# Optimization experiments

Hardware: AMD Instinct MI355X
Metric: run time of the kernel (lower is better)

## Reference

```python
import jax, jax.numpy as jnp
import numpy as np

B, S, D, M, E, K = 4, 1024, 2048, 512, 8, 2
AUX_W = 0.01


def setup_inputs() -> dict:
    key = jax.random.key(0)
    ks = jax.random.split(key, 9)
    n = lambda k, sh, fan: jax.random.normal(k, sh, jnp.float32) * (fan ** -0.5)
    return {
        "hidden_states": jax.random.normal(ks[0], (B, S, D), jnp.float32),
        "w_router": n(ks[1], (D, E), D),
        "wi0": n(ks[2], (E, D, M), D),
        "wi1": n(ks[3], (E, D, M), D),
        "wo": n(ks[4], (E, M, D), M),
        "sw_wi0": n(ks[5], (D, M), D),
        "sw_wi1": n(ks[6], (D, M), D),
        "sw_wo": n(ks[7], (M, D), M),
        "w_shared_gate": n(ks[8], (D, 1), D),
        "deterministic": 1,
    }


def reference(hidden_states, w_router, wi0, wi1, wo, sw_wi0, sw_wi1, sw_wo, w_shared_gate, deterministic):
    b, s, d = hidden_states.shape
    x = hidden_states.reshape(-1, d)  # [T, D]
    T = x.shape[0]

    # --- router: softmax over experts, top-k, renormalize top-k weights ---
    logits = (x @ w_router).astype(jnp.float32)           # [T, E]
    probs = jax.nn.softmax(logits, axis=-1)
    top_w, top_i = jax.lax.top_k(probs, K)                # [T, K]
    top_w = top_w / jnp.sum(top_w, axis=-1, keepdims=True)
    one_hot = jax.nn.one_hot(top_i, E, dtype=probs.dtype)  # [T, K, E]
    combine = jnp.einsum("tk,tke->te", top_w, one_hot)     # [T, E] sparse combine weights

    # --- load-balance aux loss (MaxText style) ---
    density = jnp.mean(jnp.sum(one_hot, axis=1), axis=0)    # fraction routed per expert
    density_proxy = jnp.mean(probs, axis=0)                 # mean router prob per expert
    load_balance_loss = jnp.mean(density * density_proxy) * (E * E) * AUX_W

    # --- routed experts: scan over experts, gated MLP, weighted combine ---
    def expert_step(acc, packed):
        wi0_e, wi1_e, wo_e, w_e = packed  # [D,M],[D,M],[M,D],[T]
        h = jax.nn.silu(x @ wi0_e) * (x @ wi1_e)            # [T, M]
        return acc + w_e[:, None] * (h @ wo_e), None

    routed, _ = jax.lax.scan(
        expert_step, jnp.zeros_like(x), (wi0, wi1, wo, combine.T)
    )

    # --- shared expert (gated MLP) + sigmoid shared gate ---
    hs = jax.nn.silu(x @ sw_wi0) * (x @ sw_wi1)
    shared = hs @ sw_wo                                     # [T, D]
    gate = jax.nn.sigmoid(x @ w_shared_gate)                # [T, 1]

    out = (routed + gate * shared).reshape(b, s, d)
    return out, load_balance_loss
```

## Files before the change

### kernel.cpp

```cpp
#include <hip/hip_runtime.h>
#include <hip/hip_bf16.h>
#include <math.h>

#define TT 4096
#define DD 2048
#define MM 512
#define EE 8

typedef __attribute__((ext_vector_type(8))) short short8;
typedef __attribute__((ext_vector_type(4))) float f32x4;

__device__ __forceinline__ unsigned short f2bf(float f) {
  union { float f; unsigned u; } v; v.f = f;
  unsigned u = v.u;
  unsigned r = u + 0x7FFFu + ((u >> 16) & 1u);
  return (unsigned short)(r >> 16);
}

__device__ __forceinline__ float bf2f(unsigned short u) {
  union { unsigned u; float f; } v; v.u = ((unsigned)u) << 16;
  return v.f;
}

__device__ __forceinline__ int imin(int a, int b) { return a < b ? a : b; }

__device__ __forceinline__ void gld16(const void* g, void* l) {
  __builtin_amdgcn_global_load_lds(
      (const __attribute__((address_space(1))) void*)g,
      (__attribute__((address_space(3))) void*)l, 16, 0, 0);
}

__global__ __launch_bounds__(256) void prep_kernel(
    const float* __restrict__ wi0, const float* __restrict__ wi1,
    const float* __restrict__ wo, const float* __restrict__ swi0,
    const float* __restrict__ swi1, const float* __restrict__ swo,
    unsigned short* __restrict__ wi0T, unsigned short* __restrict__ wi1T,
    unsigned short* __restrict__ woT, unsigned short* __restrict__ swi0T,
    unsigned short* __restrict__ swi1T, unsigned short* __restrict__ swoT,
    const float* __restrict__ x, const float* __restrict__ wr,
    const float* __restrict__ wg, unsigned short* __restrict__ xb,
    int* __restrict__ topk_i, float* __restrict__ topk_w,
    float* __restrict__ gate, int* __restrict__ cnt, float* __restrict__ proxy)
{
  __shared__ unsigned short st[64][72];
  __shared__ float s_proxy[EE];
  __shared__ int s_cnt[EE];
  int b = blockIdx.x;
  int tid = threadIdx.x;

  if (b < 27 * 64) {
    int slice = b >> 6, q = b & 63;
    const float* s; unsigned short* d;
    int R, C, tcb;
    if (slice < 8)       { s = wi0 + (size_t)slice * DD * MM;        d = wi0T + (size_t)slice * DD * MM;        R = DD; C = MM; tcb = 3; }
    else if (slice < 16) { s = wi1 + (size_t)(slice - 8) * DD * MM;  d = wi1T + (size_t)(slice - 8) * DD * MM;  R = DD; C = MM; tcb = 3; }
    else if (slice < 24) { s = wo + (size_t)(slice - 16) * MM * DD;  d = woT + (size_t)(slice - 16) * MM * DD;  R = MM; C = DD; tcb = 5; }
    else if (slice == 24){ s = swi0; d = swi0T; R = DD; C = MM; tcb = 3; }
    else if (slice == 25){ s = swi1; d = swi1T; R = DD; C = MM; tcb = 3; }
    else                 { s = swo;  d = swoT;  R = MM; C = DD; tcb = 5; }
    int ncmask = (1 << tcb) - 1;
    int tr = tid >> 4;
    int tc4 = (tid & 15) * 4;
    int orow = tid >> 2;
    int oc = (tid & 3) * 16;

    float4 cur[4], nxt[4];
    int t0 = q * 4;
    int c0 = (t0 & ncmask) * 64, r0 = (t0 >> tcb) * 64;
#pragma unroll
    for (int i = 0; i < 4; ++i)
      cur[i] = *(const float4*)&s[(size_t)(r0 + tr + i * 16) * C + (c0 + tc4)];

    for (int k = 0; k < 4; ++k) {
      int nr0 = 0, nc0 = 0;
      if (k < 3) {
        int t = q * 4 + k + 1;
        nc0 = (t & ncmask) * 64; nr0 = (t >> tcb) * 64;
#pragma unroll
        for (int i = 0; i < 4; ++i)
          nxt[i] = *(const float4*)&s[(size_t)(nr0 + tr + i * 16) * C + (nc0 + tc4)];
      }
      __builtin_amdgcn_s_barrier();
#pragma unroll
      for (int i = 0; i < 4; ++i) {
        int r = tr + i * 16;
        st[r][tc4 + 0] = f2bf(cur[i].x); st[r][tc4 + 1] = f2bf(cur[i].y);
        st[r][tc4 + 2] = f2bf(cur[i].z); st[r][tc4 + 3] = f2bf(cur[i].w);
      }
      asm volatile("s_waitcnt lgkmcnt(0)" ::: "memory");
      __builtin_amdgcn_s_barrier();
      short8 v0, v1;
#pragma unroll
      for (int j = 0; j < 8; ++j) { v0[j] = st[oc + j][orow]; v1[j] = st[oc + 8 + j][orow]; }
      *(short8*)&d[(size_t)(c0 + orow) * R + (r0 + oc)] = v0;
      *(short8*)&d[(size_t)(c0 + orow) * R + (r0 + oc + 8)] = v1;
      if (k < 3) {
        r0 = nr0; c0 = nc0;
#pragma unroll
        for (int i = 0; i < 4; ++i) cur[i] = nxt[i];
      }
    }
    return;
  }

  int rb = b - 27 * 64;
  if (tid < EE) { s_proxy[tid] = 0.f; s_cnt[tid] = 0; }
  __syncthreads();
  int wave = tid >> 6, lane = tid & 63;
  int t = rb * 4 + wave;
  const float* xr = x + (size_t)t * DD;
  unsigned short* xbr = xb + (size_t)t * DD;
  float p[EE];
#pragma unroll
  for (int e = 0; e < EE; ++e) p[e] = 0.f;
  float pg = 0.f;
  for (int i = 0; i < DD / 64; ++i) {
    int d = lane + i * 64;
    float xv = xr[d];
    xbr[d] = f2bf(xv);
    const float* w = wr + d * EE;
#pragma unroll
    for (int e = 0; e < EE; ++e) p[e] = fmaf(xv, w[e], p[e]);
    pg = fmaf(xv, wg[d], pg);
  }
#pragma unroll
  for (int e = 0; e < EE; ++e) {
#pragma unroll
    for (int off = 32; off; off >>= 1) p[e] += __shfl_xor(p[e], off);
  }
#pragma unroll
  for (int off = 32; off; off >>= 1) pg += __shfl_xor(pg, off);

  if (lane == 0) {
    float mx = p[0];
#pragma unroll
    for (int e = 1; e < EE; ++e) mx = fmaxf(mx, p[e]);
    float pr[EE]; float s = 0.f;
#pragma unroll
    for (int e = 0; e < EE; ++e) { pr[e] = __expf(p[e] - mx); s += pr[e]; }
    float inv = 1.f / s;
#pragma unroll
    for (int e = 0; e < EE; ++e) pr[e] *= inv;
    int i0 = 0;
#pragma unroll
    for (int e = 1; e < EE; ++e) if (p[e] > p[i0]) i0 = e;
    int i1 = (i0 == 0) ? 1 : 0;
#pragma unroll
    for (int e = 0; e < EE; ++e) if (e != i0 && p[e] > p[i1]) i1 = e;
    float w0 = pr[i0], w1 = pr[i1], s2 = w0 + w1;
    topk_i[t * 2] = i0; topk_i[t * 2 + 1] = i1;
    topk_w[t * 2] = w0 / s2; topk_w[t * 2 + 1] = w1 / s2;
    gate[t] = 1.f / (1.f + __expf(-pg));
    atomicAdd(&s_cnt[i0], 1);
    atomicAdd(&s_cnt[i1], 1);
#pragma unroll
    for (int e = 0; e < EE; ++e) atomicAdd(&s_proxy[e], pr[e]);
  }
  __syncthreads();
  if (tid < EE) {
    atomicAdd(&cnt[tid], s_cnt[tid]);
    atomicAdd(&proxy[tid], s_proxy[tid]);
  }
}

__global__ void offsets_loss_kernel(const int* __restrict__ cnt, int* __restrict__ offs,
                                    const float* __restrict__ proxy, float* __restrict__ out_loss)
{
  if (threadIdx.x == 0 && blockIdx.x == 0) {
    int acc = 0; float l = 0.f;
    for (int e = 0; e < EE; ++e) {
      offs[e] = acc; acc += cnt[e];
      l += (float)cnt[e] * proxy[e];
    }
    out_loss[0] = l * (0.01f * (float)EE) / ((float)TT * (float)TT);
  }
}

__global__ void fill_kernel(const int* __restrict__ topk_i,
                            const int* __restrict__ offs, int* __restrict__ fillc,
                            int* __restrict__ btok, int* __restrict__ slotOf)
{
  int idx = blockIdx.x * blockDim.x + threadIdx.x;
  if (idx >= TT * 2) return;
  int e = topk_i[idx];
  int slot = atomicAdd(&fillc[e], 1);
  int p = offs[e] + slot;
  btok[p] = idx >> 1;
  slotOf[idx] = p;
}

__global__ __launch_bounds__(256) void gemm1_kernel(
    const unsigned short* __restrict__ xb,
    const unsigned short* __restrict__ wi0T, const unsigned short* __restrict__ wi1T,
    const unsigned short* __restrict__ swi0T, const unsigned short* __restrict__ swi1T,
    unsigned short* __restrict__ H, unsigned short* __restrict__ Hs,
    const int* __restrict__ btok, const int* __restrict__ cnt, const int* __restrict__ offs)
{
  __shared__ __align__(16) unsigned short lA0[128 * 64];
  __shared__ __align__(16) unsigned short lA1[128 * 64];
  __shared__ __align__(16) unsigned short lB0[128 * 64];
  __shared__ __align__(16) unsigned short lB1[128 * 64];
  int z = blockIdx.z;
  const unsigned short *w0, *w1;
  const int* tok = nullptr;
  unsigned short* Ho;
  int n;
  if (z < EE) {
    n = cnt[z];
    int rb = offs[z];
    tok = btok + rb;
    w0 = wi0T + (size_t)z * (DD * MM);
    w1 = wi1T + (size_t)z * (DD * MM);
    Ho = H + (size_t)rb * MM;
  } else { n = TT; w0 = swi0T; w1 = swi1T; Ho = Hs; }
  int row0 = blockIdx.y * 128;
  if (row0 >= n) return;
  int m0 = blockIdx.x * 64;
  int tid = threadIdx.x, lane = tid & 63, wv = tid >> 6;

  int lsub = lane >> 3;
  int chl = (lane & 7) ^ lsub;

  const unsigned short* gA[4];
  const unsigned short* gB[4];
#pragma unroll
  for (int c = 0; c < 4; ++c) {
    int row = c * 32 + wv * 8 + lsub;
    int tr;
    if (tok) tr = tok[imin(row0 + row, n - 1)];
    else     tr = row0 + row;
    gA[c] = xb + (size_t)tr * DD + chl * 8;
    int mat = row >> 6, col = row & 63;
    const unsigned short* wsel = mat ? w1 : w0;
    gB[c] = wsel + (size_t)(m0 + col) * DD + chl * 8;
  }

  int rw = (wv & 1) * 64;
  int cg = (wv >> 1) * 32;
  int fr = lane & 15;
  int grp = lane >> 4;
  int lr4 = (lane >> 4) * 4, lc = lane & 15;

  f32x4 acc[4][4];
  f32x4 zf = {0.f, 0.f, 0.f, 0.f};
#pragma unroll
  for (int i = 0; i < 4; ++i)
#pragma unroll
    for (int c = 0; c < 4; ++c) acc[i][c] = zf;

  auto stage = [&](int kk, unsigned short* la, unsigned short* lb) {
#pragma unroll
    for (int c = 0; c < 4; ++c) gld16(gA[c] + kk, la + c * 2048 + wv * 512);
#pragma unroll
    for (int c = 0; c < 4; ++c) gld16(gB[c] + kk, lb + c * 2048 + wv * 512);
  };
  auto compute = [&](const unsigned short* la, const unsigned short* lb) {
#pragma unroll
    for (int s = 0; s < 2; ++s) {
      int cq = s * 4 + grp;
      short8 af[4], bf[4];
#pragma unroll
      for (int i = 0; i < 4; ++i) {
        int row = rw + i * 16 + fr;
        af[i] = *(const short8*)&la[row * 64 + ((cq ^ (row & 7)) * 8)];
      }
#pragma unroll
      for (int c = 0; c < 4; ++c) {
        int rowb = (c >> 1) * 64 + cg + (c & 1) * 16 + fr;
        bf[c] = *(const short8*)&lb[rowb * 64 + ((cq ^ (rowb & 7)) * 8)];
      }
#pragma unroll
      for (int i = 0; i < 4; ++i)
#pragma unroll
        for (int c = 0; c < 4; ++c)
          acc[i][c] = __builtin_amdgcn_mfma_f32_16x16x32_bf16(af[i], bf[c], acc[i][c], 0, 0, 0);
    }
  };

  stage(0, lA0, lB0);
  __syncthreads();

  int k0 = 0;
  for (; k0 < DD - 128; k0 += 128) {
    stage(k0 + 64, lA1, lB1);
    compute(lA0, lB0);
    __syncthreads();
    stage(k0 + 128, lA0, lB0);
    compute(lA1, lB1);
    __syncthreads();
  }
  stage(k0 + 64, lA1, lB1);
  compute(lA0, lB0);
  __syncthreads();
  compute(lA1, lB1);

#pragma unroll
  for (int i = 0; i < 4; ++i) {
#pragma unroll
    for (int c = 0; c < 2; ++c) {
#pragma unroll
      for (int rg = 0; rg < 4; ++rg) {
        int row = row0 + rw + i * 16 + lr4 + rg;
        if (row < n) {
          float a0 = acc[i][c][rg];
          float a1 = acc[i][c + 2][rg];
          float h = a0 / (1.f + __expf(-a0)) * a1;
          Ho[(size_t)row * MM + m0 + cg + c * 16 + lc] = f2bf(h);
        }
      }
    }
  }
}

__global__ __launch_bounds__(256) void gemm2_kernel(
    const unsigned short* __restrict__ H, const unsigned short* __restrict__ Hs,
    const unsigned short* __restrict__ woT, const unsigned short* __restrict__ swoT,
    unsigned short* __restrict__ Yr, unsigned short* __restrict__ Ys,
    const int* __restrict__ cnt, const int* __restrict__ offs)
{
  __shared__ __align__(16) unsigned short lA0[128 * 64];
  __shared__ __align__(16) unsigned short lA1[128 * 64];
  __shared__ __align__(16) unsigned short lB0[128 * 64];
  __shared__ __align__(16) unsigned short lB1[128 * 64];
  int z = blockIdx.z;
  int n, rb;
  const unsigned short *Hb, *wb;
  unsigned short* Yd;
  if (z < EE) { n = cnt[z]; rb = offs[z]; Hb = H + (size_t)rb * MM; wb = woT + (size_t)z * (DD * MM); Yd = Yr + (size_t)rb * DD; }
  else        { n = TT; rb = 0; Hb = Hs; wb = swoT; Yd = Ys; }
  int row0 = blockIdx.y * 128;
  if (row0 >= n) return;
  int d0 = blockIdx.x * 128;
  int tid = threadIdx.x, lane = tid & 63, wv = tid >> 6;

  int lsub = lane >> 3;
  int chl = (lane & 7) ^ lsub;

  const unsigned short* gA[4];
  const unsigned short* gB[4];
#pragma unroll
  for (int c = 0; c < 4; ++c) {
    int row = c * 32 + wv * 8 + lsub;
    int sr = imin(row0 + row, n - 1);
    gA[c] = Hb + (size_t)sr * MM + chl * 8;
    gB[c] = wb + (size_t)(d0 + row) * MM + chl * 8;
  }

  int rw = (wv & 1) * 64;
  int cw = (wv >> 1) * 64;
  int fr = lane & 15;
  int grp = lane >> 4;
  int lr4 = (lane >> 4) * 4, lc = lane & 15;

  f32x4 acc[4][4];
  f32x4 zf = {0.f, 0.f, 0.f, 0.f};
#pragma unroll
  for (int i = 0; i < 4; ++i)
#pragma unroll
    for (int c = 0; c < 4; ++c) acc[i][c] = zf;

  auto stage = [&](int kk, unsigned short* la, unsigned short* lb) {
#pragma unroll
    for (int c = 0; c < 4; ++c) gld16(gA[c] + kk, la + c * 2048 + wv * 512);
#pragma unroll
    for (int c = 0; c < 4; ++c) gld16(gB[c] + kk, lb + c * 2048 + wv * 512);
  };
  auto compute = [&](const unsigned short* la, const unsigned short* lb) {
#pragma unroll
    for (int s = 0; s < 2; ++s) {
      int cq = s * 4 + grp;
      short8 af[4], bf[4];
#pragma unroll
      for (int i = 0; i < 4; ++i) {
        int row = rw + i * 16 + fr;
        af[i] = *(const short8*)&la[row * 64 + ((cq ^ (row & 7)) * 8)];
      }
#pragma unroll
      for (int c = 0; c < 4; ++c) {
        int rowb = cw + c * 16 + fr;
        bf[c] = *(const short8*)&lb[rowb * 64 + ((cq ^ (rowb & 7)) * 8)];
      }
#pragma unroll
      for (int i = 0; i < 4; ++i)
#pragma unroll
        for (int c = 0; c < 4; ++c)
          acc[i][c] = __builtin_amdgcn_mfma_f32_16x16x32_bf16(af[i], bf[c], acc[i][c], 0, 0, 0);
    }
  };

  stage(0, lA0, lB0);
  __syncthreads();

  int k0 = 0;
  for (; k0 < MM - 128; k0 += 128) {
    stage(k0 + 64, lA1, lB1);
    compute(lA0, lB0);
    __syncthreads();
    stage(k0 + 128, lA0, lB0);
    compute(lA1, lB1);
    __syncthreads();
  }
  stage(k0 + 64, lA1, lB1);
  compute(lA0, lB0);
  __syncthreads();
  compute(lA1, lB1);

#pragma unroll
  for (int i = 0; i < 4; ++i) {
#pragma unroll
    for (int c = 0; c < 4; ++c) {
#pragma unroll
      for (int rg = 0; rg < 4; ++rg) {
        int row = row0 + rw + i * 16 + lr4 + rg;
        if (row < n)
          Yd[(size_t)row * DD + d0 + cw + c * 16 + lc] = f2bf(acc[i][c][rg]);
      }
    }
  }
}

__global__ __launch_bounds__(256) void combine_kernel(
    const unsigned short* __restrict__ Yr, const unsigned short* __restrict__ Ys,
    const int* __restrict__ slotOf, const float* __restrict__ topk_w,
    const float* __restrict__ gate, float* __restrict__ out)
{
  int t = blockIdx.x;
  int d0 = threadIdx.x * 8;
  int p0 = slotOf[t * 2], p1 = slotOf[t * 2 + 1];
  float w0 = topk_w[t * 2], w1 = topk_w[t * 2 + 1], g = gate[t];
  short8 a = *(const short8*)&Yr[(size_t)p0 * DD + d0];
  short8 b = *(const short8*)&Yr[(size_t)p1 * DD + d0];
  short8 s = *(const short8*)&Ys[(size_t)t * DD + d0];
  float r[8];
#pragma unroll
  for (int j = 0; j < 8; ++j)
    r[j] = w0 * bf2f((unsigned short)a[j]) + w1 * bf2f((unsigned short)b[j])
         + g * bf2f((unsigned short)s[j]);
  float4 o0 = {r[0], r[1], r[2], r[3]};
  float4 o1 = {r[4], r[5], r[6], r[7]};
  float* op = out + (size_t)t * DD + d0;
  *(float4*)op = o0;
  *(float4*)(op + 4) = o1;
}

extern "C" void kernel_launch(void* const* d_in, const int* in_sizes, int n_in,
                              void* d_out, int out_size, void* d_ws, size_t ws_size,
                              hipStream_t stream) {
  const float* x    = (const float*)d_in[0];
  const float* wr   = (const float*)d_in[1];
  const float* wi0  = (const float*)d_in[2];
  const float* wi1  = (const float*)d_in[3];
  const float* wo   = (const float*)d_in[4];
  const float* swi0 = (const float*)d_in[5];
  const float* swi1 = (const float*)d_in[6];
  const float* swo  = (const float*)d_in[7];
  const float* wg   = (const float*)d_in[8];
  float* out = (float*)d_out;

  char* ws = (char*)d_ws;
  int*   cnt    = (int*)(ws + 0);
  int*   fillc  = (int*)(ws + 64);
  int*   offs   = (int*)(ws + 128);
  float* proxy  = (float*)(ws + 192);
  int*   topk_i = (int*)(ws + 1024);
  float* topk_w = (float*)(ws + 33792);
  int*   btok   = (int*)(ws + 66560);
  float* gate   = (float*)(ws + 132096);
  int*   slotOf = (int*)(ws + 148480);
  unsigned short* xb    = (unsigned short*)(ws + 1048576);
  unsigned short* H     = (unsigned short*)(ws + 17825792);
  unsigned short* Hs    = (unsigned short*)(ws + 26214400);
  unsigned short* wi0T  = (unsigned short*)(ws + 30408704);
  unsigned short* wi1T  = (unsigned short*)(ws + 47185920);
  unsigned short* woT   = (unsigned short*)(ws + 63963136);
  unsigned short* swi0T = (unsigned short*)(ws + 80740352);
  unsigned short* swi1T = (unsigned short*)(ws + 82837504);
  unsigned short* swoT  = (unsigned short*)(ws + 84934656);
  unsigned short* Ys = xb;
  unsigned short* Yr = wi0T;

  hipMemsetAsync(ws, 0, 256, stream);

  prep_kernel<<<27 * 64 + TT / 4, 256, 0, stream>>>(
      wi0, wi1, wo, swi0, swi1, swo, wi0T, wi1T, woT, swi0T, swi1T, swoT,
      x, wr, wg, xb, topk_i, topk_w, gate, cnt, proxy);
  offsets_loss_kernel<<<1, 64, 0, stream>>>(cnt, offs, proxy, out + (size_t)TT * DD);
  fill_kernel<<<(TT * 2) / 256, 256, 0, stream>>>(topk_i, offs, fillc, btok, slotOf);

  gemm1_kernel<<<dim3(MM / 64, 32, EE + 1), 256, 0, stream>>>(
      xb, wi0T, wi1T, swi0T, swi1T, H, Hs, btok, cnt, offs);
  gemm2_kernel<<<dim3(DD / 128, 32, EE + 1), 256, 0, stream>>>(
      H, Hs, woT, swoT, Yr, Ys, cnt, offs);
  combine_kernel<<<TT, 256, 0, stream>>>(Yr, Ys, slotOf, topk_w, gate, out);
}
```

Before: 218.4 us.

## Keep two LDS stages in flight with partial vmcnt waits and raw barriers

```diff
diff --git a/kernel.cpp b/kernel.cpp
--- a/kernel.cpp
+++ b/kernel.cpp
@@ -9,6 +9,8 @@
 
 typedef __attribute__((ext_vector_type(8))) short short8;
 typedef __attribute__((ext_vector_type(4))) float f32x4;
+
+#define BARRIER() asm volatile("s_barrier" ::: "memory")
 
 __device__ __forceinline__ unsigned short f2bf(float f) {
   union { float f; unsigned u; } v; v.f = f;
@@ -278,20 +280,27 @@
   };
 
   stage(0, lA0, lB0);
-  __syncthreads();
-
-  int k0 = 0;
-  for (; k0 < DD - 128; k0 += 128) {
-    stage(k0 + 64, lA1, lB1);
+  stage(64, lA1, lB1);
+  asm volatile("s_waitcnt vmcnt(8)" ::: "memory");
+  BARRIER();
+
+#pragma unroll 1
+  for (int j = 0; j < DD / 128 - 1; ++j) {
+    int k0 = j * 128;
     compute(lA0, lB0);
-    __syncthreads();
+    BARRIER();
     stage(k0 + 128, lA0, lB0);
+    asm volatile("s_waitcnt vmcnt(8)" ::: "memory");
+    BARRIER();
     compute(lA1, lB1);
-    __syncthreads();
-  }
-  stage(k0 + 64, lA1, lB1);
+    BARRIER();
+    stage(k0 + 192, lA1, lB1);
+    asm volatile("s_waitcnt vmcnt(8)" ::: "memory");
+    BARRIER();
+  }
   compute(lA0, lB0);
-  __syncthreads();
+  asm volatile("s_waitcnt vmcnt(0)" ::: "memory");
+  BARRIER();
   compute(lA1, lB1);
 
 #pragma unroll
@@ -389,20 +398,27 @@
   };
 
   stage(0, lA0, lB0);
-  __syncthreads();
-
-  int k0 = 0;
-  for (; k0 < MM - 128; k0 += 128) {
-    stage(k0 + 64, lA1, lB1);
+  stage(64, lA1, lB1);
+  asm volatile("s_waitcnt vmcnt(8)" ::: "memory");
+  BARRIER();
+
+#pragma unroll 1
+  for (int j = 0; j < MM / 128 - 1; ++j) {
+    int k0 = j * 128;
     compute(lA0, lB0);
-    __syncthreads();
+    BARRIER();
     stage(k0 + 128, lA0, lB0);
+    asm volatile("s_waitcnt vmcnt(8)" ::: "memory");
+    BARRIER();
     compute(lA1, lB1);
-    __syncthreads();
-  }
-  stage(k0 + 64, lA1, lB1);
+    BARRIER();
+    stage(k0 + 192, lA1, lB1);
+    asm volatile("s_waitcnt vmcnt(8)" ::: "memory");
+    BARRIER();
+  }
   compute(lA0, lB0);
-  __syncthreads();
+  asm volatile("s_waitcnt vmcnt(0)" ::: "memory");
+  BARRIER();
   compute(lA1, lB1);
 
 #pragma unroll
```

Measured after the change: 219.6 us. Within noise of the previous version (+0.5%).
